# Kernel tuning notes

Hardware: AMD Instinct MI355X
Metric: run time of the kernel (lower is better)

## Reference

```python
import jax, jax.numpy as jnp
import numpy as np

KS = 4
STRIDE = 2
PAD = 1
PI = 3.14  # module uses 3.14, not math.pi


def gabor_filters(freq, theta, psi, sigma):
    # freq/theta/psi/sigma: [O, I] -> weight [O, I, KS, KS]
    x0 = float(np.ceil(KS / 2))  # 2.0 for KS=4
    lin = jnp.linspace(-x0 + 1.0, x0, KS)  # [-1, 0, 1, 2]
    y = lin[:, None]  # varies along kernel dim 0 (meshgrid 'ij')
    x = lin[None, :]  # varies along kernel dim 1
    f = freq[..., None, None]
    t = theta[..., None, None]
    p = psi[..., None, None]
    s = sigma[..., None, None]
    rotx = x * jnp.cos(t) + y * jnp.sin(t)
    roty = -x * jnp.sin(t) + y * jnp.cos(t)
    g = jnp.exp(-0.5 * (rotx ** 2 + roty ** 2) / (s + 0.001) ** 2)
    g = g * jnp.cos(f * rotx + p)
    return g / (2.0 * PI * s ** 2)


def setup_inputs() -> dict:
    key = jax.random.key(0)
    ks = jax.random.split(key, 5)
    B, I, O, H, W = 32, 64, 128, 128, 128
    x = jax.random.normal(ks[0], (B, I, H, W), dtype=jnp.float32)
    # parameter init mirroring the torch module
    freq = (PI / 2) * 1.41 ** (-jax.random.randint(ks[1], (O, I), 0, 5).astype(jnp.float32))
    theta = (PI / 8) * jax.random.randint(ks[2], (O, I), 0, 8).astype(jnp.float32)
    psi = PI * jax.random.uniform(ks[3], (O, I), dtype=jnp.float32)
    sigma = PI / freq
    gamma = jnp.ones((O,), dtype=jnp.float32)
    beta = jnp.zeros((O,), dtype=jnp.float32)
    return {"x": x, "freq": freq, "theta": theta, "psi": psi,
            "sigma": sigma, "gamma": gamma, "beta": beta}


def reference(x, freq, theta, psi, sigma, gamma, beta):
    w = gabor_filters(freq, theta, psi, sigma)  # [O, I, 4, 4]
    out = jax.lax.conv_general_dilated(
        x, w, window_strides=(STRIDE, STRIDE),
        padding=[(PAD, PAD), (PAD, PAD)],
        dimension_numbers=("NCHW", "OIHW", "NCHW"))
    # BatchNorm2d in training mode: batch stats over (N, H, W), eps=1e-5
    mean = jnp.mean(out, axis=(0, 2, 3), keepdims=True)
    var = jnp.var(out, axis=(0, 2, 3), keepdims=True)
    xhat = (out - mean) * jax.lax.rsqrt(var + 1e-5)
    out = gamma[None, :, None, None] * xhat + beta[None, :, None, None]
    # LeakyReLU(0.1)
    return jnp.where(out >= 0, out, 0.1 * out)
```

## Files before the change

### kernel.cpp

```cpp
#include <hip/hip_runtime.h>
#include <hip/hip_bf16.h>

#define BATCH 32
#define CIN   64
#define COUT  128
#define HIN   128
#define WIN   128
#define HOUT  64
#define WOUT  64

typedef unsigned int u32;
typedef unsigned short u16;
typedef __attribute__((ext_vector_type(8))) short short8;
typedef __attribute__((ext_vector_type(4))) float f32x4;


__device__ inline u16 f2bf(float v) {
  __hip_bfloat16 h = __float2bfloat16(v);
  return *reinterpret_cast<u16*>(&h);
}
__device__ inline u32 pack2(float a, float b) {
  return (u32)f2bf(a) | ((u32)f2bf(b) << 16);
}

__global__ __launch_bounds__(256) void gabor_kernel(
    const float* __restrict__ freq, const float* __restrict__ theta,
    const float* __restrict__ psi,  const float* __restrict__ sigma,
    __hip_bfloat16* __restrict__ wsw) {
  int idx = blockIdx.x * 256 + threadIdx.x;
  int o = idx >> 6, i = idx & 63;
  float f = freq[idx], t = theta[idx], p = psi[idx], s = sigma[idx];
  float ct = cosf(t), st = sinf(t);
  float se = s + 0.001f;
  float gsc = -0.5f / (se * se);
  float nrm = 1.0f / (2.0f * 3.14f * s * s);
  const float lin[4] = {-1.f, 0.f, 1.f, 2.f};
  int chunk = i >> 2, i4 = i & 3;
  #pragma unroll
  for (int ky = 0; ky < 4; ++ky) {
    #pragma unroll
    for (int kx = 0; kx < 4; ++kx) {
      float xx = lin[kx], yy = lin[ky];
      float rx =  xx * ct + yy * st;
      float ry = -xx * st + yy * ct;
      float g = __expf(gsc * (rx * rx + ry * ry)) * cosf(f * rx + p) * nrm;
      int sub = 4 * (i4 >> 1) + ky;
      int j = 2 * kx + (i4 & 1);
      int slot = sub ^ (o & 7);
      wsw[(chunk * 16384 + o * 128 + slot * 16 + j * 2) >> 1] = __float2bfloat16(g);
    }
  }
}

constexpr int XRLEN  = 136;
constexpr int XROWS  = 18;
constexpr int XPLANE = 2448;
constexpr int XBYTES = 19584;
constexpr int NSLOT  = 1152;

__global__ __launch_bounds__(1024, 4) void conv_mfma(
    const float* __restrict__ x, const char* __restrict__ wsW,
    float* __restrict__ out, u16* __restrict__ outb,
    float2* __restrict__ part) {
  __shared__ __align__(16) char lds[71936];

  const int tid = threadIdx.x;
  const int l = tid & 63, w = tid >> 6;
  const int wm = w & 1, wn = w >> 1;
  const int t4 = l >> 4, lcol = l & 15;
  const int ohb = blockIdx.x, b = blockIdx.y;
  const int oh0 = ohb * 8;

  bool act[2]; int xdw[2]; const float* gpA[2];
  #pragma unroll
  for (int u = 0; u < 2; ++u) {
    int sg = tid + u * 1024;
    int p = sg / 576, rem = sg - p * 576;
    int r = rem >> 5, s = rem & 31;
    int ih = oh0 * 2 - 1 + r;
    act[u] = (sg < NSLOT) && ((unsigned)ih < 128u);
    xdw[u] = p * XPLANE + r * XRLEN + 4 * s + 3;
    int ch = 2 * p;
    gpA[u] = x + (((size_t)(b * 64 + ch) << 14) + (size_t)ih * 128 + 4 * s);
  }

  float4 xva[2], xvb[2];
  auto XLOAD = [&](int c) {
    #pragma unroll
    for (int u = 0; u < 2; ++u)
      if (act[u]) {
        const float* p = gpA[u] + (size_t)c * 65536;
        xva[u] = *(const float4*)p;
        xvb[u] = *(const float4*)(p + 16384);
      }
  };
  auto XWRITE = [&](int nb) {
    u32* X = (u32*)(lds + 32768 + nb * XBYTES);
    #pragma unroll
    for (int u = 0; u < 2; ++u)
      if (act[u]) {
        u32 w0 = pack2(xva[u].x, xvb[u].x);
        u32 w1 = pack2(xva[u].y, xvb[u].y);
        u32 w2 = pack2(xva[u].z, xvb[u].z);
        u32 w3 = pack2(xva[u].w, xvb[u].w);
        X[xdw[u]] = w0;
        uint2 mid; mid.x = w1; mid.y = w2;
        *(uint2*)(X + xdw[u] + 1) = mid;
        X[xdw[u] + 3] = w3;
      }
  };

  auto ASTAGE = [&](int c, int nb) {
    const char* src = wsW + c * 16384 + w * 1024 + l * 16;
    char* dst = lds + nb * 16384 + w * 1024;
    __builtin_amdgcn_global_load_lds(
        (const __attribute__((address_space(1))) u32*)src,
        (__attribute__((address_space(3))) u32*)dst, 16, 0, 0);
  };

  {
    u32* X = (u32*)(lds + 32768);
    for (int i = tid; i < 2 * XBYTES / 4; i += 1024) X[i] = 0;
  }

  f32x4 acc[4][4];
  #pragma unroll
  for (int mf = 0; mf < 4; ++mf)
    #pragma unroll
    for (int nf = 0; nf < 4; ++nf) acc[mf][nf] = {0.f, 0.f, 0.f, 0.f};

  int bo[4];
  #pragma unroll
  for (int nf = 0; nf < 4; ++nf) {
    int nfb = 4 * wn + nf;
    int owt = ((nfb & 3) << 4) + lcol;
    bo[nf] = (2 * (nfb >> 2) + t4) * XRLEN + 2 * owt + 2;
  }

  int ao[4][2];
  #pragma unroll
  for (int mf = 0; mf < 4; ++mf)
    #pragma unroll
    for (int kk = 0; kk < 2; ++kk)
      ao[mf][kk] = (wm * 64 + mf * 16 + lcol) * 128 +
                   (((4 * kk + t4) ^ (lcol & 7)) << 4);

  auto COMPUTE = [&](int cb) {
    const char* Ab = lds + cb * 16384;
    const u32* Xb = (const u32*)(lds + 32768 + cb * XBYTES);
    __builtin_amdgcn_s_setprio(1);
    #pragma unroll
    for (int kk = 0; kk < 2; ++kk) {
      short8 af[4];
      #pragma unroll
      for (int mf = 0; mf < 4; ++mf)
        af[mf] = *(const short8*)(Ab + ao[mf][kk]);
      #pragma unroll
      for (int nf = 0; nf < 4; ++nf) {
        const u32* q = Xb + bo[nf] + kk * XPLANE;
        union { uint2 u2[2]; short8 s8; } bu;
        bu.u2[0] = *(const uint2*)(q);
        bu.u2[1] = *(const uint2*)(q + 2);
        short8 bf = bu.s8;
        #pragma unroll
        for (int mf = 0; mf < 4; ++mf)
          acc[mf][nf] = __builtin_amdgcn_mfma_f32_16x16x32_bf16(af[mf], bf, acc[mf][nf], 0, 0, 0);
      }
    }
    __builtin_amdgcn_s_setprio(0);
  };

  ASTAGE(0, 0); XLOAD(0);
  __syncthreads();
  XWRITE(0);
  __syncthreads();
  for (int c = 0; c < 16; ++c) {
    int cur = c & 1;
    if (c < 15) { ASTAGE(c + 1, cur ^ 1); XLOAD(c + 1); }
    COMPUTE(cur);
    if (c < 15) XWRITE(cur ^ 1);
    __syncthreads();
  }

  size_t obase = ((size_t)b * 128) * 4096;
  if (outb) {
    #pragma unroll
    for (int mf = 0; mf < 4; ++mf)
      #pragma unroll
      for (int nf = 0; nf < 4; ++nf) {
        int nfb = 4 * wn + nf;
        int oh = oh0 + (nfb >> 2), ow = ((nfb & 3) << 4) + lcol;
        #pragma unroll
        for (int r = 0; r < 4; ++r) {
          int o = wm * 64 + mf * 16 + t4 * 4 + r;
          outb[obase + (size_t)o * 4096 + oh * 64 + ow] = f2bf(acc[mf][nf][r]);
        }
      }
  } else {
    #pragma unroll
    for (int mf = 0; mf < 4; ++mf)
      #pragma unroll
      for (int nf = 0; nf < 4; ++nf) {
        int nfb = 4 * wn + nf;
        int oh = oh0 + (nfb >> 2), ow = ((nfb & 3) << 4) + lcol;
        #pragma unroll
        for (int r = 0; r < 4; ++r) {
          int o = wm * 64 + mf * 16 + t4 * 4 + r;
          out[obase + (size_t)o * 4096 + oh * 64 + ow] = acc[mf][nf][r];
        }
      }
  }

  float* ps = (float*)lds;
  #pragma unroll
  for (int mf = 0; mf < 4; ++mf)
    #pragma unroll
    for (int r = 0; r < 4; ++r) {
      float s1 = 0.f, s2 = 0.f;
      #pragma unroll
      for (int nf = 0; nf < 4; ++nf) { float v = acc[mf][nf][r]; s1 += v; s2 += v * v; }
      #pragma unroll
      for (int d = 1; d < 16; d <<= 1) { s1 += __shfl_xor(s1, d); s2 += __shfl_xor(s2, d); }
      if (lcol == 0) {
        int o = wm * 64 + mf * 16 + t4 * 4 + r;
        ps[o * 16 + wn * 2 + 0] = s1;
        ps[o * 16 + wn * 2 + 1] = s2;
      }
    }
  __syncthreads();
  if (tid < 128) {
    float s1 = 0.f, s2 = 0.f;
    #pragma unroll
    for (int q = 0; q < 8; ++q) {
      s1 += ps[tid * 16 + q * 2 + 0];
      s2 += ps[tid * 16 + q * 2 + 1];
    }
    part[(size_t)tid * 256 + b * 8 + ohb] = make_float2(s1, s2);
  }
}

__global__ __launch_bounds__(256) void stats_kernel(
    const float2* __restrict__ part, const float* __restrict__ gamma,
    const float* __restrict__ beta, float2* __restrict__ ab) {
  int o = blockIdx.x;
  int tid = threadIdx.x;
  float2 p = part[(size_t)o * 256 + tid];
  float s1 = p.x, s2 = p.y;
  __shared__ float r1[256], r2[256];
  r1[tid] = s1; r2[tid] = s2;
  __syncthreads();
  for (int off = 128; off > 0; off >>= 1) {
    if (tid < off) { r1[tid] += r1[tid + off]; r2[tid] += r2[tid + off]; }
    __syncthreads();
  }
  if (tid == 0) {
    const float N = (float)BATCH * HOUT * WOUT;
    float mean = r1[0] / N;
    float var  = r2[0] / N - mean * mean;
    float inv  = rsqrtf(var + 1e-5f);
    float a = gamma[o] * inv;
    float bb = beta[o] - mean * a;
    ab[o] = make_float2(a, bb);
  }
}

__global__ __launch_bounds__(256) void norm_bf16_kernel(
    const u32* __restrict__ cb, const float2* __restrict__ ab,
    float* __restrict__ out) {
  size_t g = (size_t)blockIdx.x * 256 + threadIdx.x;
  int o = (int)((g >> 9) & (COUT - 1));
  float2 s = ab[o];
  uint4 pk = ((const uint4*)cb)[g];
  float e[8];
  e[0] = __uint_as_float(pk.x << 16); e[1] = __uint_as_float(pk.x & 0xffff0000u);
  e[2] = __uint_as_float(pk.y << 16); e[3] = __uint_as_float(pk.y & 0xffff0000u);
  e[4] = __uint_as_float(pk.z << 16); e[5] = __uint_as_float(pk.z & 0xffff0000u);
  e[6] = __uint_as_float(pk.w << 16); e[7] = __uint_as_float(pk.w & 0xffff0000u);
  #pragma unroll
  for (int i = 0; i < 8; ++i) {
    float v = fmaf(e[i], s.x, s.y);
    e[i] = v >= 0.f ? v : 0.1f * v;
  }
  float4* op = (float4*)(out + g * 8);
  op[0] = make_float4(e[0], e[1], e[2], e[3]);
  op[1] = make_float4(e[4], e[5], e[6], e[7]);
}

__global__ __launch_bounds__(256) void norm_kernel(
    float* __restrict__ out, const float2* __restrict__ ab) {
  size_t idx = (size_t)blockIdx.x * 256 + threadIdx.x;
  int o = (int)((idx >> 10) & (COUT - 1));
  float2 s = ab[o];
  float4 v = reinterpret_cast<float4*>(out)[idx];
  v.x = fmaf(v.x, s.x, s.y);
  v.y = fmaf(v.y, s.x, s.y);
  v.z = fmaf(v.z, s.x, s.y);
  v.w = fmaf(v.w, s.x, s.y);
  v.x = v.x >= 0.f ? v.x : 0.1f * v.x;
  v.y = v.y >= 0.f ? v.y : 0.1f * v.y;
  v.z = v.z >= 0.f ? v.z : 0.1f * v.z;
  v.w = v.w >= 0.f ? v.w : 0.1f * v.w;
  reinterpret_cast<float4*>(out)[idx] = v;
}

extern "C" void kernel_launch(void* const* d_in, const int* in_sizes, int n_in,
                              void* d_out, int out_size, void* d_ws, size_t ws_size,
                              hipStream_t stream) {
  const float* x     = (const float*)d_in[0];
  const float* freq  = (const float*)d_in[1];
  const float* theta = (const float*)d_in[2];
  const float* psi   = (const float*)d_in[3];
  const float* sigma = (const float*)d_in[4];
  const float* gamma = (const float*)d_in[5];
  const float* beta  = (const float*)d_in[6];
  float* out = (float*)d_out;

  __hip_bfloat16* wsw = (__hip_bfloat16*)d_ws;
  float2* part = (float2*)((char*)d_ws + 262144);
  float2* ab   = (float2*)((char*)d_ws + 786432);

  const size_t WSO_OFF = 1048576;
  const size_t WSO_BYTES = (size_t)BATCH * COUT * HOUT * WOUT * 2;
  bool fast = ws_size >= WSO_OFF + WSO_BYTES;
  u16* wsO = fast ? (u16*)((char*)d_ws + WSO_OFF) : nullptr;

  gabor_kernel<<<32, 256, 0, stream>>>(freq, theta, psi, sigma, wsw);
  conv_mfma<<<dim3(8, BATCH), 1024, 0, stream>>>(x, (const char*)d_ws, out, wsO, part);
  stats_kernel<<<COUT, 256, 0, stream>>>(part, gamma, beta, ab);
  if (fast)
    norm_bf16_kernel<<<2097152 / 256, 256, 0, stream>>>((const u32*)wsO, ab, out);
  else
    norm_kernel<<<4194304 / 256, 256, 0, stream>>>(out, ab);
}
```

Baseline: 74.82 us.

## Double conv K-chunk per stage and fuse BN stats into normalize kernel

The conv kernel now stages 8 input channels per pipeline step instead of 4. That halves the number of loop iterations and barriers, doubles the LDS footprint to about 140KB, and changes the weight layout and swizzle to match. The separate stats kernel is folded into the bf16 normalize kernel: each block recomputes its channel's mean and variance from the partial sums, which removes one launch and the round-trip through the ab buffer. The cost is redundant per-block reductions and higher LDS use, which can limit residency of the conv blocks.

```diff
diff --git a/kernel.cpp b/kernel.cpp
--- a/kernel.cpp
+++ b/kernel.cpp
@@ -35,7 +35,9 @@
   float gsc = -0.5f / (se * se);
   float nrm = 1.0f / (2.0f * 3.14f * s * s);
   const float lin[4] = {-1.f, 0.f, 1.f, 2.f};
-  int chunk = i >> 2, i4 = i & 3;
+  int chunk = i >> 3;
+  int kk = (i & 7) >> 1;
+  int parity = i & 1;
   #pragma unroll
   for (int ky = 0; ky < 4; ++ky) {
     #pragma unroll
@@ -44,10 +46,9 @@
       float rx =  xx * ct + yy * st;
       float ry = -xx * st + yy * ct;
       float g = __expf(gsc * (rx * rx + ry * ry)) * cosf(f * rx + p) * nrm;
-      int sub = 4 * (i4 >> 1) + ky;
-      int j = 2 * kx + (i4 & 1);
-      int slot = sub ^ (o & 7);
-      wsw[(chunk * 16384 + o * 128 + slot * 16 + j * 2) >> 1] = __float2bfloat16(g);
+      int slot = (4 * kk + ky) ^ (o & 15);
+      wsw[(chunk * 32768 + o * 256 + slot * 16 + (2 * kx + parity) * 2) >> 1] =
+          __float2bfloat16(g);
     }
   }
 }
@@ -55,14 +56,14 @@
 constexpr int XRLEN  = 136;
 constexpr int XROWS  = 18;
 constexpr int XPLANE = 2448;
-constexpr int XBYTES = 19584;
-constexpr int NSLOT  = 1152;
+constexpr int XBYTES = 39168;
+constexpr int NSLOT  = 2304;
 
 __global__ __launch_bounds__(1024, 4) void conv_mfma(
     const float* __restrict__ x, const char* __restrict__ wsW,
     float* __restrict__ out, u16* __restrict__ outb,
     float2* __restrict__ part) {
-  __shared__ __align__(16) char lds[71936];
+  __shared__ __align__(16) char lds[143872];
 
   const int tid = threadIdx.x;
   const int l = tid & 63, w = tid >> 6;
@@ -71,9 +72,9 @@
   const int ohb = blockIdx.x, b = blockIdx.y;
   const int oh0 = ohb * 8;
 
-  bool act[2]; int xdw[2]; const float* gpA[2];
-  #pragma unroll
-  for (int u = 0; u < 2; ++u) {
+  bool act[3]; int xdw[3]; const float* gpA[3];
+  #pragma unroll
+  for (int u = 0; u < 3; ++u) {
     int sg = tid + u * 1024;
     int p = sg / 576, rem = sg - p * 576;
     int r = rem >> 5, s = rem & 31;
@@ -84,20 +85,20 @@
     gpA[u] = x + (((size_t)(b * 64 + ch) << 14) + (size_t)ih * 128 + 4 * s);
   }
 
-  float4 xva[2], xvb[2];
+  float4 xva[3], xvb[3];
   auto XLOAD = [&](int c) {
     #pragma unroll
-    for (int u = 0; u < 2; ++u)
+    for (int u = 0; u < 3; ++u)
       if (act[u]) {
-        const float* p = gpA[u] + (size_t)c * 65536;
+        const float* p = gpA[u] + (size_t)c * 131072;
         xva[u] = *(const float4*)p;
         xvb[u] = *(const float4*)(p + 16384);
       }
   };
   auto XWRITE = [&](int nb) {
-    u32* X = (u32*)(lds + 32768 + nb * XBYTES);
-    #pragma unroll
-    for (int u = 0; u < 2; ++u)
+    u32* X = (u32*)(lds + 65536 + nb * XBYTES);
+    #pragma unroll
+    for (int u = 0; u < 3; ++u)
       if (act[u]) {
         u32 w0 = pack2(xva[u].x, xvb[u].x);
         u32 w1 = pack2(xva[u].y, xvb[u].y);
@@ -111,15 +112,18 @@
   };
 
   auto ASTAGE = [&](int c, int nb) {
-    const char* src = wsW + c * 16384 + w * 1024 + l * 16;
-    char* dst = lds + nb * 16384 + w * 1024;
+    const char* src = wsW + c * 32768 + w * 2048 + l * 16;
+    char* dst = lds + nb * 32768 + w * 2048;
     __builtin_amdgcn_global_load_lds(
         (const __attribute__((address_space(1))) u32*)src,
         (__attribute__((address_space(3))) u32*)dst, 16, 0, 0);
+    __builtin_amdgcn_global_load_lds(
+        (const __attribute__((address_space(1))) u32*)(src + 1024),
+        (__attribute__((address_space(3))) u32*)(dst + 1024), 16, 0, 0);
   };
 
   {
-    u32* X = (u32*)(lds + 32768);
+    u32* X = (u32*)(lds + 65536);
     for (int i = tid; i < 2 * XBYTES / 4; i += 1024) X[i] = 0;
   }
 
@@ -137,20 +141,20 @@
     bo[nf] = (2 * (nfb >> 2) + t4) * XRLEN + 2 * owt + 2;
   }
 
-  int ao[4][2];
+  int ao[4][4];
   #pragma unroll
   for (int mf = 0; mf < 4; ++mf)
     #pragma unroll
-    for (int kk = 0; kk < 2; ++kk)
-      ao[mf][kk] = (wm * 64 + mf * 16 + lcol) * 128 +
-                   (((4 * kk + t4) ^ (lcol & 7)) << 4);
+    for (int kk = 0; kk < 4; ++kk)
+      ao[mf][kk] = (wm * 64 + mf * 16 + lcol) * 256 +
+                   (((4 * kk + t4) ^ lcol) << 4);
 
   auto COMPUTE = [&](int cb) {
-    const char* Ab = lds + cb * 16384;
-    const u32* Xb = (const u32*)(lds + 32768 + cb * XBYTES);
+    const char* Ab = lds + cb * 32768;
+    const u32* Xb = (const u32*)(lds + 65536 + cb * XBYTES);
     __builtin_amdgcn_s_setprio(1);
     #pragma unroll
-    for (int kk = 0; kk < 2; ++kk) {
+    for (int kk = 0; kk < 4; ++kk) {
       short8 af[4];
       #pragma unroll
       for (int mf = 0; mf < 4; ++mf)
@@ -174,11 +178,11 @@
   __syncthreads();
   XWRITE(0);
   __syncthreads();
-  for (int c = 0; c < 16; ++c) {
+  for (int c = 0; c < 8; ++c) {
     int cur = c & 1;
-    if (c < 15) { ASTAGE(c + 1, cur ^ 1); XLOAD(c + 1); }
+    if (c < 7) { ASTAGE(c + 1, cur ^ 1); XLOAD(c + 1); }
     COMPUTE(cur);
-    if (c < 15) XWRITE(cur ^ 1);
+    if (c < 7) XWRITE(cur ^ 1);
     __syncthreads();
   }
 
@@ -237,6 +241,47 @@
     }
     part[(size_t)tid * 256 + b * 8 + ohb] = make_float2(s1, s2);
   }
+}
+
+__global__ __launch_bounds__(256) void norm_stats_bf16_kernel(
+    const u32* __restrict__ cb, const float2* __restrict__ part,
+    const float* __restrict__ gamma, const float* __restrict__ beta,
+    float* __restrict__ out) {
+  const int tid = threadIdx.x;
+  const int l = tid & 63, w = tid >> 6;
+  const int o = (blockIdx.x >> 1) & (COUT - 1);
+
+  float2 pv = part[(size_t)o * 256 + tid];
+  float s1 = pv.x, s2 = pv.y;
+  #pragma unroll
+  for (int d = 1; d < 64; d <<= 1) { s1 += __shfl_xor(s1, d); s2 += __shfl_xor(s2, d); }
+  __shared__ float psum[8];
+  if (l == 0) { psum[w * 2] = s1; psum[w * 2 + 1] = s2; }
+  __syncthreads();
+  float t1 = psum[0] + psum[2] + psum[4] + psum[6];
+  float t2 = psum[1] + psum[3] + psum[5] + psum[7];
+  const float N = (float)BATCH * HOUT * WOUT;
+  float mean = t1 / N;
+  float var  = t2 / N - mean * mean;
+  float inv  = rsqrtf(var + 1e-5f);
+  float a  = gamma[o] * inv;
+  float bb = beta[o] - mean * a;
+
+  size_t g = (size_t)blockIdx.x * 256 + tid;
+  uint4 pk = ((const uint4*)cb)[g];
+  float e[8];
+  e[0] = __uint_as_float(pk.x << 16); e[1] = __uint_as_float(pk.x & 0xffff0000u);
+  e[2] = __uint_as_float(pk.y << 16); e[3] = __uint_as_float(pk.y & 0xffff0000u);
+  e[4] = __uint_as_float(pk.z << 16); e[5] = __uint_as_float(pk.z & 0xffff0000u);
+  e[6] = __uint_as_float(pk.w << 16); e[7] = __uint_as_float(pk.w & 0xffff0000u);
+  #pragma unroll
+  for (int i = 0; i < 8; ++i) {
+    float v = fmaf(e[i], a, bb);
+    e[i] = v >= 0.f ? v : 0.1f * v;
+  }
+  float4* op = (float4*)(out + g * 8);
+  op[0] = make_float4(e[0], e[1], e[2], e[3]);
+  op[1] = make_float4(e[4], e[5], e[6], e[7]);
 }
 
 __global__ __launch_bounds__(256) void stats_kernel(
@@ -262,28 +307,6 @@
     float bb = beta[o] - mean * a;
     ab[o] = make_float2(a, bb);
   }
-}
-
-__global__ __launch_bounds__(256) void norm_bf16_kernel(
-    const u32* __restrict__ cb, const float2* __restrict__ ab,
-    float* __restrict__ out) {
-  size_t g = (size_t)blockIdx.x * 256 + threadIdx.x;
-  int o = (int)((g >> 9) & (COUT - 1));
-  float2 s = ab[o];
-  uint4 pk = ((const uint4*)cb)[g];
-  float e[8];
-  e[0] = __uint_as_float(pk.x << 16); e[1] = __uint_as_float(pk.x & 0xffff0000u);
-  e[2] = __uint_as_float(pk.y << 16); e[3] = __uint_as_float(pk.y & 0xffff0000u);
-  e[4] = __uint_as_float(pk.z << 16); e[5] = __uint_as_float(pk.z & 0xffff0000u);
-  e[6] = __uint_as_float(pk.w << 16); e[7] = __uint_as_float(pk.w & 0xffff0000u);
-  #pragma unroll
-  for (int i = 0; i < 8; ++i) {
-    float v = fmaf(e[i], s.x, s.y);
-    e[i] = v >= 0.f ? v : 0.1f * v;
-  }
-  float4* op = (float4*)(out + g * 8);
-  op[0] = make_float4(e[0], e[1], e[2], e[3]);
-  op[1] = make_float4(e[4], e[5], e[6], e[7]);
 }
 
 __global__ __launch_bounds__(256) void norm_kernel(
@@ -326,9 +349,11 @@
 
   gabor_kernel<<<32, 256, 0, stream>>>(freq, theta, psi, sigma, wsw);
   conv_mfma<<<dim3(8, BATCH), 1024, 0, stream>>>(x, (const char*)d_ws, out, wsO, part);
-  stats_kernel<<<COUT, 256, 0, stream>>>(part, gamma, beta, ab);
-  if (fast)
-    norm_bf16_kernel<<<2097152 / 256, 256, 0, stream>>>((const u32*)wsO, ab, out);
-  else
+  if (fast) {
+    norm_stats_bf16_kernel<<<2097152 / 256, 256, 0, stream>>>(
+        (const u32*)wsO, part, gamma, beta, out);
+  } else {
+    stats_kernel<<<COUT, 256, 0, stream>>>(part, gamma, beta, ab);
     norm_kernel<<<4194304 / 256, 256, 0, stream>>>(out, ab);
-}
+  }
+}
```

Measured after the change: 75.20 us. No clear change (+0.5%).

## Halve conv tile height to double grid and fuse BN stats into normalize

Applied to the files above, without the earlier changes.

The conv kernel now covers 4 output rows per block with 512 threads instead of 8 rows with 1024 threads. That doubles the grid to 512 blocks and shrinks LDS, which should give better occupancy and CU coverage on a 256-CU part. Each wave stages twice as much weight data. The separate stats kernel is folded into the bf16 normalize kernel: every block redundantly reduces the 512 partial sums for its channel, which removes a launch and the serial dependency at the cost of repeated small reductions.

```diff
diff --git a/kernel.cpp b/kernel.cpp
--- a/kernel.cpp
+++ b/kernel.cpp
@@ -53,29 +53,29 @@
 }
 
 constexpr int XRLEN  = 136;
-constexpr int XROWS  = 18;
-constexpr int XPLANE = 2448;
-constexpr int XBYTES = 19584;
-constexpr int NSLOT  = 1152;
-
-__global__ __launch_bounds__(1024, 4) void conv_mfma(
+constexpr int XROWS  = 10;
+constexpr int XPLANE = 1360;
+constexpr int XBYTES = 10880;
+constexpr int NSLOT  = 640;
+
+__global__ __launch_bounds__(512, 4) void conv_mfma(
     const float* __restrict__ x, const char* __restrict__ wsW,
     float* __restrict__ out, u16* __restrict__ outb,
     float2* __restrict__ part) {
-  __shared__ __align__(16) char lds[71936];
+  __shared__ __align__(16) char lds[54528];
 
   const int tid = threadIdx.x;
   const int l = tid & 63, w = tid >> 6;
   const int wm = w & 1, wn = w >> 1;
   const int t4 = l >> 4, lcol = l & 15;
   const int ohb = blockIdx.x, b = blockIdx.y;
-  const int oh0 = ohb * 8;
+  const int oh0 = ohb * 4;
 
   bool act[2]; int xdw[2]; const float* gpA[2];
   #pragma unroll
   for (int u = 0; u < 2; ++u) {
-    int sg = tid + u * 1024;
-    int p = sg / 576, rem = sg - p * 576;
+    int sg = tid + u * 512;
+    int p = sg / 320, rem = sg - p * 320;
     int r = rem >> 5, s = rem & 31;
     int ih = oh0 * 2 - 1 + r;
     act[u] = (sg < NSLOT) && ((unsigned)ih < 128u);
@@ -111,16 +111,19 @@
   };
 
   auto ASTAGE = [&](int c, int nb) {
-    const char* src = wsW + c * 16384 + w * 1024 + l * 16;
-    char* dst = lds + nb * 16384 + w * 1024;
+    const char* src = wsW + c * 16384 + w * 2048 + l * 16;
+    char* dst = lds + nb * 16384 + w * 2048;
     __builtin_amdgcn_global_load_lds(
         (const __attribute__((address_space(1))) u32*)src,
         (__attribute__((address_space(3))) u32*)dst, 16, 0, 0);
+    __builtin_amdgcn_global_load_lds(
+        (const __attribute__((address_space(1))) u32*)(src + 1024),
+        (__attribute__((address_space(3))) u32*)(dst + 1024), 16, 0, 0);
   };
 
   {
     u32* X = (u32*)(lds + 32768);
-    for (int i = tid; i < 2 * XBYTES / 4; i += 1024) X[i] = 0;
+    for (int i = tid; i < 2 * XBYTES / 4; i += 512) X[i] = 0;
   }
 
   f32x4 acc[4][4];
@@ -223,20 +226,62 @@
       for (int d = 1; d < 16; d <<= 1) { s1 += __shfl_xor(s1, d); s2 += __shfl_xor(s2, d); }
       if (lcol == 0) {
         int o = wm * 64 + mf * 16 + t4 * 4 + r;
-        ps[o * 16 + wn * 2 + 0] = s1;
-        ps[o * 16 + wn * 2 + 1] = s2;
+        ps[o * 8 + wn * 2 + 0] = s1;
+        ps[o * 8 + wn * 2 + 1] = s2;
       }
     }
   __syncthreads();
   if (tid < 128) {
     float s1 = 0.f, s2 = 0.f;
     #pragma unroll
-    for (int q = 0; q < 8; ++q) {
-      s1 += ps[tid * 16 + q * 2 + 0];
-      s2 += ps[tid * 16 + q * 2 + 1];
+    for (int q = 0; q < 4; ++q) {
+      s1 += ps[tid * 8 + q * 2 + 0];
+      s2 += ps[tid * 8 + q * 2 + 1];
     }
-    part[(size_t)tid * 256 + b * 8 + ohb] = make_float2(s1, s2);
-  }
+    part[(size_t)tid * 512 + b * 16 + ohb] = make_float2(s1, s2);
+  }
+}
+
+__global__ __launch_bounds__(256) void norm_stats_bf16_kernel(
+    const u32* __restrict__ cb, const float2* __restrict__ part,
+    const float* __restrict__ gamma, const float* __restrict__ beta,
+    float* __restrict__ out) {
+  const int tid = threadIdx.x;
+  const int l = tid & 63, w = tid >> 6;
+  const int o = (blockIdx.x >> 1) & (COUT - 1);
+
+  float2 p0 = part[(size_t)o * 512 + tid];
+  float2 p1 = part[(size_t)o * 512 + tid + 256];
+  float s1 = p0.x + p1.x, s2 = p0.y + p1.y;
+  #pragma unroll
+  for (int d = 1; d < 64; d <<= 1) { s1 += __shfl_xor(s1, d); s2 += __shfl_xor(s2, d); }
+  __shared__ float psum[8];
+  if (l == 0) { psum[w * 2] = s1; psum[w * 2 + 1] = s2; }
+  __syncthreads();
+  float t1 = psum[0] + psum[2] + psum[4] + psum[6];
+  float t2 = psum[1] + psum[3] + psum[5] + psum[7];
+  const float N = (float)BATCH * HOUT * WOUT;
+  float mean = t1 / N;
+  float var  = t2 / N - mean * mean;
+  float inv  = rsqrtf(var + 1e-5f);
+  float a  = gamma[o] * inv;
+  float bb = beta[o] - mean * a;
+
+  size_t g = (size_t)blockIdx.x * 256 + tid;
+  uint4 pk = ((const uint4*)cb)[g];
+  float e[8];
+  e[0] = __uint_as_float(pk.x << 16); e[1] = __uint_as_float(pk.x & 0xffff0000u);
+  e[2] = __uint_as_float(pk.y << 16); e[3] = __uint_as_float(pk.y & 0xffff0000u);
+  e[4] = __uint_as_float(pk.z << 16); e[5] = __uint_as_float(pk.z & 0xffff0000u);
+  e[6] = __uint_as_float(pk.w << 16); e[7] = __uint_as_float(pk.w & 0xffff0000u);
+  #pragma unroll
+  for (int i = 0; i < 8; ++i) {
+    float v = fmaf(e[i], a, bb);
+    e[i] = v >= 0.f ? v : 0.1f * v;
+  }
+  float4* op = (float4*)(out + g * 8);
+  op[0] = make_float4(e[0], e[1], e[2], e[3]);
+  op[1] = make_float4(e[4], e[5], e[6], e[7]);
 }
 
 __global__ __launch_bounds__(256) void stats_kernel(
@@ -244,8 +289,12 @@
     const float* __restrict__ beta, float2* __restrict__ ab) {
   int o = blockIdx.x;
   int tid = threadIdx.x;
-  float2 p = part[(size_t)o * 256 + tid];
-  float s1 = p.x, s2 = p.y;
+  float s1 = 0.f, s2 = 0.f;
+  #pragma unroll
+  for (int t = 0; t < 2; ++t) {
+    float2 p = part[(size_t)o * 512 + tid + t * 256];
+    s1 += p.x; s2 += p.y;
+  }
   __shared__ float r1[256], r2[256];
   r1[tid] = s1; r2[tid] = s2;
   __syncthreads();
@@ -262,28 +311,6 @@
     float bb = beta[o] - mean * a;
     ab[o] = make_float2(a, bb);
   }
-}
-
-__global__ __launch_bounds__(256) void norm_bf16_kernel(
-    const u32* __restrict__ cb, const float2* __restrict__ ab,
-    float* __restrict__ out) {
-  size_t g = (size_t)blockIdx.x * 256 + threadIdx.x;
-  int o = (int)((g >> 9) & (COUT - 1));
-  float2 s = ab[o];
-  uint4 pk = ((const uint4*)cb)[g];
-  float e[8];
-  e[0] = __uint_as_float(pk.x << 16); e[1] = __uint_as_float(pk.x & 0xffff0000u);
-  e[2] = __uint_as_float(pk.y << 16); e[3] = __uint_as_float(pk.y & 0xffff0000u);
-  e[4] = __uint_as_float(pk.z << 16); e[5] = __uint_as_float(pk.z & 0xffff0000u);
-  e[6] = __uint_as_float(pk.w << 16); e[7] = __uint_as_float(pk.w & 0xffff0000u);
-  #pragma unroll
-  for (int i = 0; i < 8; ++i) {
-    float v = fmaf(e[i], s.x, s.y);
-    e[i] = v >= 0.f ? v : 0.1f * v;
-  }
-  float4* op = (float4*)(out + g * 8);
-  op[0] = make_float4(e[0], e[1], e[2], e[3]);
-  op[1] = make_float4(e[4], e[5], e[6], e[7]);
 }
 
 __global__ __launch_bounds__(256) void norm_kernel(
@@ -325,10 +352,12 @@
   u16* wsO = fast ? (u16*)((char*)d_ws + WSO_OFF) : nullptr;
 
   gabor_kernel<<<32, 256, 0, stream>>>(freq, theta, psi, sigma, wsw);
-  conv_mfma<<<dim3(8, BATCH), 1024, 0, stream>>>(x, (const char*)d_ws, out, wsO, part);
-  stats_kernel<<<COUT, 256, 0, stream>>>(part, gamma, beta, ab);
-  if (fast)
-    norm_bf16_kernel<<<2097152 / 256, 256, 0, stream>>>((const u32*)wsO, ab, out);
-  else
+  conv_mfma<<<dim3(16, BATCH), 512, 0, stream>>>(x, (const char*)d_ws, out, wsO, part);
+  if (fast) {
+    norm_stats_bf16_kernel<<<2097152 / 256, 256, 0, stream>>>(
+        (const u32*)wsO, part, gamma, beta, out);
+  } else {
+    stats_kernel<<<COUT, 256, 0, stream>>>(part, gamma, beta, ab);
     norm_kernel<<<4194304 / 256, 256, 0, stream>>>(out, ab);
-}
+  }
+}
```

After: 70.86 us, median of 2. -5.3%, faster.
